# Performance work log

Measured on AMD Instinct MI355X. Metric: run time of the kernel, lower is better.

Reference implementation:

```python
import jax, jax.numpy as jnp
import numpy as np

NDIR = 6      # build_tree.num_directions()
IDIM = 256
ODIM = 512
B, L, NCH = 8, 4096, 8192


def setup_inputs() -> dict:
    key = jax.random.key(0)
    ks = jax.random.split(key, 9)
    last = jax.random.normal(ks[0], (B, NCH, IDIM), dtype=jnp.float32)
    child_l = jax.random.randint(ks[1], (L,), 0, NCH, dtype=jnp.int32)
    child_r = jax.random.randint(ks[2], (L,), 0, NCH, dtype=jnp.int32)
    vec = jax.random.randint(ks[3], (B, L), 0, NCH, dtype=jnp.int32)
    drev = jax.random.randint(ks[4], (NCH,), 0, 2, dtype=jnp.int32)
    dmap = jax.random.randint(ks[5], (NCH,), 0, NDIR, dtype=jnp.int32)
    # merge FC params: ndir independent Linear(2*idim -> odim) + PReLU(init=relu_weight)
    scale = 1.0 / np.sqrt(2 * IDIM)
    W_merge = jax.random.uniform(ks[6], (NDIR, ODIM, 2 * IDIM), jnp.float32, -scale, scale)
    b_merge = jax.random.uniform(ks[7], (NDIR, ODIM), jnp.float32, -scale, scale)
    alpha_merge = jnp.full((NDIR,), 0.005, dtype=jnp.float32)  # PReLU weight (relu_weight)
    return {"last": last, "W_merge": W_merge, "b_merge": b_merge,
            "alpha_merge": alpha_merge, "child_l": child_l, "child_r": child_r,
            "vec": vec, "drev": drev, "dmap": dmap}


def reference(last, W_merge, b_merge, alpha_merge, child_l, child_r, vec, drev, dmap):
    # child gathers: [B, L, idim]
    lch = last[:, child_l]
    rch = last[:, child_r]
    # per-element direction-reverse blending
    d = drev[vec][:, :, None].astype(last.dtype)          # [B, L, 1]
    a = lch * (1.0 - d) + rch * d
    b = rch * (1.0 - d) + lch * d
    ans = jnp.concatenate([a, b], axis=-1)                # [B, L, 2*idim]
    # routed merge: compute all ndir linears, then select per element (ndir is small)
    y_all = jnp.einsum('bli,doi->bldo', ans, W_merge) + b_merge   # [B, L, ndir, odim]
    dir_idx = dmap[vec]                                   # [B, L] in [0, ndir)
    y = jnp.take_along_axis(y_all, dir_idx[:, :, None, None], axis=2)[:, :, 0]  # [B, L, odim]
    alpha = alpha_merge[dir_idx][:, :, None]              # per-element PReLU slope
    return jnp.where(y > 0, y, alpha * y)
```

## Files before the change

kernel.cpp:

```cpp
#include <hip/hip_runtime.h>
#include <hip/hip_bf16.h>

#define BB 8
#define LL 4096
#define NCH 8192
#define IDIM 256
#define KDIM 512
#define ODIM 512
#define NDIR 6
#define TOT (BB * LL)
#define MT 64

typedef short short8 __attribute__((ext_vector_type(8)));
typedef float floatx4 __attribute__((ext_vector_type(4)));

#define IDX_OFF 64
#define ROWS_OFF (64 + NDIR * TOT)
#define LASTBF_OFF (64 + 2 * NDIR * TOT)
#define LAST_ELEMS (BB * NCH * IDIM)
#define W_ELEMS (NDIR * ODIM * KDIM)
#define N_LAST8 (LAST_ELEMS / 8)
#define N_W8 (W_ELEMS / 8)

__device__ inline void async_copy16(const void* g, void* l) {
  __builtin_amdgcn_global_load_lds(
      (const __attribute__((address_space(1))) void*)g,
      (__attribute__((address_space(3))) void*)l, 16, 0, 0);
}

__device__ inline void cvt8(const float* __restrict__ src,
                            __hip_bfloat16* __restrict__ dst, int i) {
  const floatx4* s = (const floatx4*)src;
  floatx4 a = s[2 * i];
  floatx4 b = s[2 * i + 1];
  union { short8 v; __hip_bfloat16 h[8]; } u;
  u.h[0] = __float2bfloat16(a[0]); u.h[1] = __float2bfloat16(a[1]);
  u.h[2] = __float2bfloat16(a[2]); u.h[3] = __float2bfloat16(a[3]);
  u.h[4] = __float2bfloat16(b[0]); u.h[5] = __float2bfloat16(b[1]);
  u.h[6] = __float2bfloat16(b[2]); u.h[7] = __float2bfloat16(b[3]);
  ((short8*)dst)[i] = u.v;
}

__global__ __launch_bounds__(256) void scatter_kernel(
    const int* __restrict__ vec, const int* __restrict__ child_l,
    const int* __restrict__ child_r, const int* __restrict__ drev,
    const int* __restrict__ dmap, int* __restrict__ ws) {
  __shared__ int lcnt[8];
  __shared__ int gbase[8];
  int tid = threadIdx.x;
  if (tid < 8) lcnt[tid] = 0;
  __syncthreads();

  int t = blockIdx.x * 256 + tid;
  int l = t & (LL - 1);
  int v = vec[t];
  int dir = dmap[v] & 7;
  int sw = drev[v];
  int cl = child_l[l];
  int cr = child_r[l];
  int r0 = sw ? cr : cl;
  int r1 = sw ? cl : cr;
  int pos = atomicAdd(&lcnt[dir], 1);
  __syncthreads();
  if (tid < 8) gbase[tid] = lcnt[tid] ? atomicAdd(&ws[tid], lcnt[tid]) : 0;
  __syncthreads();
  int slot = dir * TOT + gbase[dir] + pos;
  ws[IDX_OFF + slot] = t;
  ws[ROWS_OFF + slot] = r0 | (r1 << 16);
}

__global__ __launch_bounds__(256) void prep_kernel(
    const float* __restrict__ last, const float* __restrict__ W,
    int* __restrict__ ws) {
  __hip_bfloat16* last_bf = (__hip_bfloat16*)(ws + LASTBF_OFF);
  __hip_bfloat16* W_bf = last_bf + LAST_ELEMS;
  int gid = blockIdx.x * 256 + threadIdx.x;
  if (gid < N_LAST8) cvt8(last, last_bf, gid);
  else cvt8(W, W_bf, gid - N_LAST8);
}

__global__ __launch_bounds__(256) void gemm_kernel(
    const float* __restrict__ bias, const float* __restrict__ alpha_m,
    const int* __restrict__ ws, float* __restrict__ out) {
  __shared__ __hip_bfloat16 Als[2][MT * 32];
  __shared__ __hip_bfloat16 Bls[2][128 * 32];

  const int mt = blockIdx.y;
  const int nt = blockIdx.x;
  int d = -1, count = 0, m_base = 0;
  {
    int tb = 0;
    for (int dd = 0; dd < NDIR; ++dd) {
      int c = ws[dd];
      int ntile = (c + MT - 1) / MT;
      if (mt < tb + ntile) { d = dd; count = c; m_base = (mt - tb) * MT; break; }
      tb += ntile;
    }
  }
  if (d < 0) return;

  const __hip_bfloat16* last_bf = (const __hip_bfloat16*)(ws + LASTBF_OFF);
  const __hip_bfloat16* W_bf = last_bf + LAST_ELEMS;
  const int* idx = ws + IDX_OFF + d * TOT;
  const int* rows = ws + ROWS_OFF + d * TOT;

  const int tid = threadIdx.x;
  const int wave = __builtin_amdgcn_readfirstlane(tid >> 6);
  const int lane = tid & 63;
  const int lane15 = lane & 15;
  const int quad = lane >> 4;
  const int wm = wave >> 1;
  const int wn = wave & 1;
  const int n_blk = nt * 128;

  const int su = ((tid & 3) ^ ((tid >> 3) & 3)) * 8;
  const __hip_bfloat16* pa0;
  const __hip_bfloat16* pa1;
  {
    int r = tid >> 2;
    int lr = m_base + r;
    if (lr >= count) lr = count - 1;
    int t = idx[lr] & (TOT - 1);
    int rr = rows[lr];
    int b = t >> 12;
    int r0 = rr & (NCH - 1);
    int r1 = (rr >> 16) & (NCH - 1);
    pa0 = last_bf + (long long)(b * NCH + r0) * IDIM + su;
    pa1 = last_bf + (long long)(b * NCH + r1) * IDIM + su;
  }
  const __hip_bfloat16* pb[2];
#pragma unroll
  for (int i = 0; i < 2; ++i) {
    int rB = i * 64 + (tid >> 2);
    pb[i] = W_bf + (long long)(d * ODIM + n_blk + rB) * KDIM + su;
  }
  const int aBase = wave * 512;
  const int bBase0 = wave * 512;
  const int bBase1 = 2048 + wave * 512;

  floatx4 acc[2][4] = {};
  const int xcol = (quad ^ ((lane15 >> 1) & 3)) * 8;

  {
    async_copy16(pa0, &Als[0][aBase]);
    async_copy16(pb[0], &Bls[0][bBase0]);
    async_copy16(pb[1], &Bls[0][bBase1]);
  }

#pragma unroll
  for (int kt = 0; kt < 16; ++kt) {
    __syncthreads();
    if (kt < 15) {
      const int nb = (kt + 1) & 1;
      const int kn = kt + 1;
      const __hip_bfloat16* ga = (kn < 8) ? pa0 + kn * 32 : pa1 + (kn - 8) * 32;
      async_copy16(ga, &Als[nb][aBase]);
      async_copy16(pb[0] + kn * 32, &Bls[nb][bBase0]);
      async_copy16(pb[1] + kn * 32, &Bls[nb][bBase1]);
    }
    const int c = kt & 1;
    short8 a[2], b[4];
#pragma unroll
    for (int i = 0; i < 2; ++i)
      a[i] = *(const short8*)&Als[c][(wm * 32 + i * 16 + lane15) * 32 + xcol];
#pragma unroll
    for (int j = 0; j < 4; ++j)
      b[j] = *(const short8*)&Bls[c][(wn * 64 + j * 16 + lane15) * 32 + xcol];
#pragma unroll
    for (int i = 0; i < 2; ++i)
#pragma unroll
      for (int j = 0; j < 4; ++j)
        acc[i][j] = __builtin_amdgcn_mfma_f32_16x16x32_bf16(a[i], b[j], acc[i][j], 0, 0, 0);
  }

  const float alpha = alpha_m[d];
  float bj[4];
#pragma unroll
  for (int j = 0; j < 4; ++j)
    bj[j] = bias[d * ODIM + n_blk + wn * 64 + j * 16 + lane15];

#pragma unroll
  for (int i = 0; i < 2; ++i) {
#pragma unroll
    for (int reg = 0; reg < 4; ++reg) {
      int row_id = m_base + wm * 32 + i * 16 + quad * 4 + reg;
      if (row_id >= count) continue;
      int t = idx[row_id] & (TOT - 1);
      float* orow = out + (long long)t * ODIM + n_blk + wn * 64;
#pragma unroll
      for (int j = 0; j < 4; ++j) {
        float y = acc[i][j][reg] + bj[j];
        y = y > 0.f ? y : alpha * y;
        orow[j * 16 + lane15] = y;
      }
    }
  }
}

extern "C" void kernel_launch(void* const* d_in, const int* in_sizes, int n_in,
                              void* d_out, int out_size, void* d_ws, size_t ws_size,
                              hipStream_t stream) {
  const float* last = (const float*)d_in[0];
  const float* W = (const float*)d_in[1];
  const float* bias = (const float*)d_in[2];
  const float* alpha = (const float*)d_in[3];
  const int* child_l = (const int*)d_in[4];
  const int* child_r = (const int*)d_in[5];
  const int* vec = (const int*)d_in[6];
  const int* drev = (const int*)d_in[7];
  const int* dmap = (const int*)d_in[8];

  int* ws = (int*)d_ws;

  hipMemsetAsync(ws, 0, 32, stream);
  scatter_kernel<<<TOT / 256, 256, 0, stream>>>(vec, child_l, child_r, drev, dmap, ws);
  prep_kernel<<<(N_LAST8 + N_W8) / 256, 256, 0, stream>>>(last, W, ws);
  dim3 grid(ODIM / 128, TOT / MT + NDIR, 1);
  gemm_kernel<<<grid, 256, 0, stream>>>(bias, alpha, ws, (float*)d_out);
}
```

Before: 173.5 us.

## Convert gathered fp32 rows to bf16 in-register; drop full last conversion pass

Removes the pre-pass that converted the whole 64M-element `last` tensor to bf16. The GEMM now gathers fp32 child rows straight from global memory into registers and converts them to bf16 before the MFMA. B fragments are likewise loaded directly from global into registers with double buffering, replacing the LDS staging and barriers. The scatter and weight-conversion kernels are merged into one launch. The cost is twice the bytes per gathered A element, and each wave redundantly loads A and B without LDS sharing, which adds global/L2 traffic.

```diff
diff --git a/kernel.cpp b/kernel.cpp
--- a/kernel.cpp
+++ b/kernel.cpp
@@ -16,75 +16,57 @@
 
 #define IDX_OFF 64
 #define ROWS_OFF (64 + NDIR * TOT)
-#define LASTBF_OFF (64 + 2 * NDIR * TOT)
-#define LAST_ELEMS (BB * NCH * IDIM)
+#define WBF_OFF (64 + 2 * NDIR * TOT)
 #define W_ELEMS (NDIR * ODIM * KDIM)
-#define N_LAST8 (LAST_ELEMS / 8)
 #define N_W8 (W_ELEMS / 8)
 
-__device__ inline void async_copy16(const void* g, void* l) {
-  __builtin_amdgcn_global_load_lds(
-      (const __attribute__((address_space(1))) void*)g,
-      (__attribute__((address_space(3))) void*)l, 16, 0, 0);
-}
-
-__device__ inline void cvt8(const float* __restrict__ src,
-                            __hip_bfloat16* __restrict__ dst, int i) {
-  const floatx4* s = (const floatx4*)src;
-  floatx4 a = s[2 * i];
-  floatx4 b = s[2 * i + 1];
-  union { short8 v; __hip_bfloat16 h[8]; } u;
-  u.h[0] = __float2bfloat16(a[0]); u.h[1] = __float2bfloat16(a[1]);
-  u.h[2] = __float2bfloat16(a[2]); u.h[3] = __float2bfloat16(a[3]);
-  u.h[4] = __float2bfloat16(b[0]); u.h[5] = __float2bfloat16(b[1]);
-  u.h[6] = __float2bfloat16(b[2]); u.h[7] = __float2bfloat16(b[3]);
-  ((short8*)dst)[i] = u.v;
-}
-
-__global__ __launch_bounds__(256) void scatter_kernel(
+__global__ __launch_bounds__(256) void prep_kernel(
     const int* __restrict__ vec, const int* __restrict__ child_l,
     const int* __restrict__ child_r, const int* __restrict__ drev,
-    const int* __restrict__ dmap, int* __restrict__ ws) {
-  __shared__ int lcnt[8];
-  __shared__ int gbase[8];
+    const int* __restrict__ dmap, const float* __restrict__ W,
+    int* __restrict__ ws) {
+  int bid = blockIdx.x;
   int tid = threadIdx.x;
-  if (tid < 8) lcnt[tid] = 0;
-  __syncthreads();
-
-  int t = blockIdx.x * 256 + tid;
-  int l = t & (LL - 1);
-  int v = vec[t];
-  int dir = dmap[v] & 7;
-  int sw = drev[v];
-  int cl = child_l[l];
-  int cr = child_r[l];
-  int r0 = sw ? cr : cl;
-  int r1 = sw ? cl : cr;
-  int pos = atomicAdd(&lcnt[dir], 1);
-  __syncthreads();
-  if (tid < 8) gbase[tid] = lcnt[tid] ? atomicAdd(&ws[tid], lcnt[tid]) : 0;
-  __syncthreads();
-  int slot = dir * TOT + gbase[dir] + pos;
-  ws[IDX_OFF + slot] = t;
-  ws[ROWS_OFF + slot] = r0 | (r1 << 16);
+  if (bid < TOT / 256) {
+    __shared__ int lcnt[8];
+    __shared__ int gbase[8];
+    if (tid < 8) lcnt[tid] = 0;
+    __syncthreads();
+    int t = bid * 256 + tid;
+    int l = t & (LL - 1);
+    int v = vec[t];
+    int dir = dmap[v] & 7;
+    int sw = drev[v];
+    int cl = child_l[l];
+    int cr = child_r[l];
+    int r0 = sw ? cr : cl;
+    int r1 = sw ? cl : cr;
+    int pos = atomicAdd(&lcnt[dir], 1);
+    __syncthreads();
+    if (tid < 8) gbase[tid] = lcnt[tid] ? atomicAdd(&ws[tid], lcnt[tid]) : 0;
+    __syncthreads();
+    int slot = dir * TOT + gbase[dir] + pos;
+    ws[IDX_OFF + slot] = t;
+    ws[ROWS_OFF + slot] = r0 | (r1 << 16);
+  } else {
+    int gid = (bid - TOT / 256) * 256 + tid;
+    __hip_bfloat16* W_bf = (__hip_bfloat16*)(ws + WBF_OFF);
+    const floatx4* s = (const floatx4*)W;
+    floatx4 a = s[2 * gid];
+    floatx4 b = s[2 * gid + 1];
+    union { short8 v; __hip_bfloat16 h[8]; } u;
+    u.h[0] = __float2bfloat16(a[0]); u.h[1] = __float2bfloat16(a[1]);
+    u.h[2] = __float2bfloat16(a[2]); u.h[3] = __float2bfloat16(a[3]);
+    u.h[4] = __float2bfloat16(b[0]); u.h[5] = __float2bfloat16(b[1]);
+    u.h[6] = __float2bfloat16(b[2]); u.h[7] = __float2bfloat16(b[3]);
+    ((short8*)W_bf)[gid] = u.v;
+  }
 }
 
-__global__ __launch_bounds__(256) void prep_kernel(
-    const float* __restrict__ last, const float* __restrict__ W,
-    int* __restrict__ ws) {
-  __hip_bfloat16* last_bf = (__hip_bfloat16*)(ws + LASTBF_OFF);
-  __hip_bfloat16* W_bf = last_bf + LAST_ELEMS;
-  int gid = blockIdx.x * 256 + threadIdx.x;
-  if (gid < N_LAST8) cvt8(last, last_bf, gid);
-  else cvt8(W, W_bf, gid - N_LAST8);
-}
-
 __global__ __launch_bounds__(256) void gemm_kernel(
-    const float* __restrict__ bias, const float* __restrict__ alpha_m,
-    const int* __restrict__ ws, float* __restrict__ out) {
-  __shared__ __hip_bfloat16 Als[2][MT * 32];
-  __shared__ __hip_bfloat16 Bls[2][128 * 32];
-
+    const float* __restrict__ last, const float* __restrict__ bias,
+    const float* __restrict__ alpha_m, const int* __restrict__ ws,
+    float* __restrict__ out) {
   const int mt = blockIdx.y;
   const int nt = blockIdx.x;
   int d = -1, count = 0, m_base = 0;
@@ -99,8 +81,7 @@
   }
   if (d < 0) return;
 
-  const __hip_bfloat16* last_bf = (const __hip_bfloat16*)(ws + LASTBF_OFF);
-  const __hip_bfloat16* W_bf = last_bf + LAST_ELEMS;
+  const __hip_bfloat16* W_bf = (const __hip_bfloat16*)(ws + WBF_OFF);
   const int* idx = ws + IDX_OFF + d * TOT;
   const int* rows = ws + ROWS_OFF + d * TOT;
 
@@ -113,64 +94,70 @@
   const int wn = wave & 1;
   const int n_blk = nt * 128;
 
-  const int su = ((tid & 3) ^ ((tid >> 3) & 3)) * 8;
-  const __hip_bfloat16* pa0;
-  const __hip_bfloat16* pa1;
-  {
-    int r = tid >> 2;
-    int lr = m_base + r;
+  const float* paf0[2];
+  const float* paf1[2];
+#pragma unroll
+  for (int i = 0; i < 2; ++i) {
+    int lr = m_base + wm * 32 + i * 16 + lane15;
     if (lr >= count) lr = count - 1;
     int t = idx[lr] & (TOT - 1);
     int rr = rows[lr];
     int b = t >> 12;
     int r0 = rr & (NCH - 1);
     int r1 = (rr >> 16) & (NCH - 1);
-    pa0 = last_bf + (long long)(b * NCH + r0) * IDIM + su;
-    pa1 = last_bf + (long long)(b * NCH + r1) * IDIM + su;
-  }
-  const __hip_bfloat16* pb[2];
+    paf0[i] = last + (long long)(b * NCH + r0) * IDIM + quad * 8;
+    paf1[i] = last + (long long)(b * NCH + r1) * IDIM + quad * 8;
+  }
+  const __hip_bfloat16* pb[4];
+#pragma unroll
+  for (int j = 0; j < 4; ++j)
+    pb[j] = W_bf + (long long)(d * ODIM + n_blk + wn * 64 + j * 16 + lane15) * KDIM + quad * 8;
+
+  floatx4 acc[2][4] = {};
+
+  floatx4 ar[2][2][2];
+  short8 br[2][4];
+
 #pragma unroll
   for (int i = 0; i < 2; ++i) {
-    int rB = i * 64 + (tid >> 2);
-    pb[i] = W_bf + (long long)(d * ODIM + n_blk + rB) * KDIM + su;
-  }
-  const int aBase = wave * 512;
-  const int bBase0 = wave * 512;
-  const int bBase1 = 2048 + wave * 512;
-
-  floatx4 acc[2][4] = {};
-  const int xcol = (quad ^ ((lane15 >> 1) & 3)) * 8;
-
-  {
-    async_copy16(pa0, &Als[0][aBase]);
-    async_copy16(pb[0], &Bls[0][bBase0]);
-    async_copy16(pb[1], &Bls[0][bBase1]);
-  }
+    ar[0][i][0] = *(const floatx4*)(paf0[i]);
+    ar[0][i][1] = *(const floatx4*)(paf0[i] + 4);
+  }
+#pragma unroll
+  for (int j = 0; j < 4; ++j) br[0][j] = *(const short8*)(pb[j]);
 
 #pragma unroll
   for (int kt = 0; kt < 16; ++kt) {
-    __syncthreads();
+    const int cur = kt & 1;
+    const int nxt = cur ^ 1;
     if (kt < 15) {
-      const int nb = (kt + 1) & 1;
       const int kn = kt + 1;
-      const __hip_bfloat16* ga = (kn < 8) ? pa0 + kn * 32 : pa1 + (kn - 8) * 32;
-      async_copy16(ga, &Als[nb][aBase]);
-      async_copy16(pb[0] + kn * 32, &Bls[nb][bBase0]);
-      async_copy16(pb[1] + kn * 32, &Bls[nb][bBase1]);
-    }
-    const int c = kt & 1;
-    short8 a[2], b[4];
+#pragma unroll
+      for (int i = 0; i < 2; ++i) {
+        const float* p = (kn < 8) ? paf0[i] + kn * 32 : paf1[i] + (kn - 8) * 32;
+        ar[nxt][i][0] = *(const floatx4*)(p);
+        ar[nxt][i][1] = *(const floatx4*)(p + 4);
+      }
+#pragma unroll
+      for (int j = 0; j < 4; ++j) br[nxt][j] = *(const short8*)(pb[j] + kn * 32);
+    }
+    short8 a[2];
+#pragma unroll
+    for (int i = 0; i < 2; ++i) {
+      union { short8 v; __hip_bfloat16 h[8]; } u;
+      floatx4 x0 = ar[cur][i][0];
+      floatx4 x1 = ar[cur][i][1];
+      u.h[0] = __float2bfloat16(x0[0]); u.h[1] = __float2bfloat16(x0[1]);
+      u.h[2] = __float2bfloat16(x0[2]); u.h[3] = __float2bfloat16(x0[3]);
+      u.h[4] = __float2bfloat16(x1[0]); u.h[5] = __float2bfloat16(x1[1]);
+      u.h[6] = __float2bfloat16(x1[2]); u.h[7] = __float2bfloat16(x1[3]);
+      a[i] = u.v;
+    }
 #pragma unroll
     for (int i = 0; i < 2; ++i)
-      a[i] = *(const short8*)&Als[c][(wm * 32 + i * 16 + lane15) * 32 + xcol];
-#pragma unroll
-    for (int j = 0; j < 4; ++j)
-      b[j] = *(const short8*)&Bls[c][(wn * 64 + j * 16 + lane15) * 32 + xcol];
-#pragma unroll
-    for (int i = 0; i < 2; ++i)
 #pragma unroll
       for (int j = 0; j < 4; ++j)
-        acc[i][j] = __builtin_amdgcn_mfma_f32_16x16x32_bf16(a[i], b[j], acc[i][j], 0, 0, 0);
+        acc[i][j] = __builtin_amdgcn_mfma_f32_16x16x32_bf16(a[i], br[cur][j], acc[i][j], 0, 0, 0);
   }
 
   const float alpha = alpha_m[d];
@@ -213,8 +200,8 @@
   int* ws = (int*)d_ws;
 
   hipMemsetAsync(ws, 0, 32, stream);
-  scatter_kernel<<<TOT / 256, 256, 0, stream>>>(vec, child_l, child_r, drev, dmap, ws);
-  prep_kernel<<<(N_LAST8 + N_W8) / 256, 256, 0, stream>>>(last, W, ws);
+  prep_kernel<<<TOT / 256 + N_W8 / 256, 256, 0, stream>>>(
+      vec, child_l, child_r, drev, dmap, W, ws);
   dim3 grid(ODIM / 128, TOT / MT + NDIR, 1);
-  gemm_kernel<<<grid, 256, 0, stream>>>(bias, alpha, ws, (float*)d_out);
+  gemm_kernel<<<grid, 256, 0, stream>>>(last, bias, alpha, ws, (float*)d_out);
 }
```

Result: slower. 252.3 us (+45.5%).

## Enlarge GEMM tile to 128x128 with K=64 steps and fuse scatter into prep kernel

Applied to the files above, without the earlier changes.

The grouped GEMM tile grows from 64x128 to 128x128, and each K step is now 64 wide with an 8-way XOR swizzle. This doubles operand reuse per LDS load and halves the number of barriers per tile. Separately, the scatter and bf16-conversion kernels are merged into one launch using block-range dispatch, which removes one kernel launch. The cost is more LDS and accumulator registers per block, which can lower occupancy, plus more padding waste on the partial last tile of each direction.

```diff
diff --git a/kernel.cpp b/kernel.cpp
--- a/kernel.cpp
+++ b/kernel.cpp
@@ -9,7 +9,7 @@
 #define ODIM 512
 #define NDIR 6
 #define TOT (BB * LL)
-#define MT 64
+#define MT 128
 
 typedef short short8 __attribute__((ext_vector_type(8)));
 typedef float floatx4 __attribute__((ext_vector_type(4)));
@@ -21,6 +21,9 @@
 #define W_ELEMS (NDIR * ODIM * KDIM)
 #define N_LAST8 (LAST_ELEMS / 8)
 #define N_W8 (W_ELEMS / 8)
+#define SCAT_BLK (TOT / 256)
+#define CVTL_BLK (N_LAST8 / 256)
+#define CVTW_BLK (N_W8 / 256)
 
 __device__ inline void async_copy16(const void* g, void* l) {
   __builtin_amdgcn_global_load_lds(
@@ -41,49 +44,48 @@
   ((short8*)dst)[i] = u.v;
 }
 
-__global__ __launch_bounds__(256) void scatter_kernel(
+__global__ __launch_bounds__(256) void prep_kernel(
     const int* __restrict__ vec, const int* __restrict__ child_l,
     const int* __restrict__ child_r, const int* __restrict__ drev,
-    const int* __restrict__ dmap, int* __restrict__ ws) {
-  __shared__ int lcnt[8];
-  __shared__ int gbase[8];
-  int tid = threadIdx.x;
-  if (tid < 8) lcnt[tid] = 0;
-  __syncthreads();
-
-  int t = blockIdx.x * 256 + tid;
-  int l = t & (LL - 1);
-  int v = vec[t];
-  int dir = dmap[v] & 7;
-  int sw = drev[v];
-  int cl = child_l[l];
-  int cr = child_r[l];
-  int r0 = sw ? cr : cl;
-  int r1 = sw ? cl : cr;
-  int pos = atomicAdd(&lcnt[dir], 1);
-  __syncthreads();
-  if (tid < 8) gbase[tid] = lcnt[tid] ? atomicAdd(&ws[tid], lcnt[tid]) : 0;
-  __syncthreads();
-  int slot = dir * TOT + gbase[dir] + pos;
-  ws[IDX_OFF + slot] = t;
-  ws[ROWS_OFF + slot] = r0 | (r1 << 16);
-}
-
-__global__ __launch_bounds__(256) void prep_kernel(
-    const float* __restrict__ last, const float* __restrict__ W,
-    int* __restrict__ ws) {
+    const int* __restrict__ dmap, const float* __restrict__ last,
+    const float* __restrict__ W, int* __restrict__ ws) {
   __hip_bfloat16* last_bf = (__hip_bfloat16*)(ws + LASTBF_OFF);
   __hip_bfloat16* W_bf = last_bf + LAST_ELEMS;
-  int gid = blockIdx.x * 256 + threadIdx.x;
-  if (gid < N_LAST8) cvt8(last, last_bf, gid);
-  else cvt8(W, W_bf, gid - N_LAST8);
-}
-
-__global__ __launch_bounds__(256) void gemm_kernel(
+  int bid = blockIdx.x;
+  int tid = threadIdx.x;
+  if (bid < SCAT_BLK) {
+    __shared__ int lcnt[8];
+    __shared__ int gbase[8];
+    if (tid < 8) lcnt[tid] = 0;
+    __syncthreads();
+    int t = bid * 256 + tid;
+    int l = t & (LL - 1);
+    int v = vec[t];
+    int dir = dmap[v] & 7;
+    int sw = drev[v];
+    int cl = child_l[l];
+    int cr = child_r[l];
+    int r0 = sw ? cr : cl;
+    int r1 = sw ? cl : cr;
+    int pos = atomicAdd(&lcnt[dir], 1);
+    __syncthreads();
+    if (tid < 8) gbase[tid] = lcnt[tid] ? atomicAdd(&ws[tid], lcnt[tid]) : 0;
+    __syncthreads();
+    int slot = dir * TOT + gbase[dir] + pos;
+    ws[IDX_OFF + slot] = t;
+    ws[ROWS_OFF + slot] = r0 | (r1 << 16);
+  } else if (bid < SCAT_BLK + CVTL_BLK) {
+    cvt8(last, last_bf, (bid - SCAT_BLK) * 256 + tid);
+  } else {
+    cvt8(W, W_bf, (bid - SCAT_BLK - CVTL_BLK) * 256 + tid);
+  }
+}
+
+__global__ __launch_bounds__(256, 2) void gemm_kernel(
     const float* __restrict__ bias, const float* __restrict__ alpha_m,
     const int* __restrict__ ws, float* __restrict__ out) {
-  __shared__ __hip_bfloat16 Als[2][MT * 32];
-  __shared__ __hip_bfloat16 Bls[2][128 * 32];
+  __shared__ __hip_bfloat16 Als[2][128 * 64];
+  __shared__ __hip_bfloat16 Bls[2][128 * 64];
 
   const int mt = blockIdx.y;
   const int nt = blockIdx.x;
@@ -113,64 +115,67 @@
   const int wn = wave & 1;
   const int n_blk = nt * 128;
 
-  const int su = ((tid & 3) ^ ((tid >> 3) & 3)) * 8;
-  const __hip_bfloat16* pa0;
-  const __hip_bfloat16* pa1;
-  {
-    int r = tid >> 2;
-    int lr = m_base + r;
+  const __hip_bfloat16* ap0[4];
+  const __hip_bfloat16* ap1[4];
+  const __hip_bfloat16* bp[4];
+  int ldsrow[4];
+#pragma unroll
+  for (int i = 0; i < 4; ++i) {
+    int sr = wave * 32 + i * 8 + (lane >> 3);
+    ldsrow[i] = (wave * 32 + i * 8) * 64;
+    int lr = m_base + sr;
     if (lr >= count) lr = count - 1;
     int t = idx[lr] & (TOT - 1);
     int rr = rows[lr];
     int b = t >> 12;
     int r0 = rr & (NCH - 1);
     int r1 = (rr >> 16) & (NCH - 1);
-    pa0 = last_bf + (long long)(b * NCH + r0) * IDIM + su;
-    pa1 = last_bf + (long long)(b * NCH + r1) * IDIM + su;
-  }
-  const __hip_bfloat16* pb[2];
-#pragma unroll
-  for (int i = 0; i < 2; ++i) {
-    int rB = i * 64 + (tid >> 2);
-    pb[i] = W_bf + (long long)(d * ODIM + n_blk + rB) * KDIM + su;
-  }
-  const int aBase = wave * 512;
-  const int bBase0 = wave * 512;
-  const int bBase1 = 2048 + wave * 512;
-
-  floatx4 acc[2][4] = {};
-  const int xcol = (quad ^ ((lane15 >> 1) & 3)) * 8;
-
-  {
-    async_copy16(pa0, &Als[0][aBase]);
-    async_copy16(pb[0], &Bls[0][bBase0]);
-    async_copy16(pb[1], &Bls[0][bBase1]);
-  }
-
-#pragma unroll
-  for (int kt = 0; kt < 16; ++kt) {
-    __syncthreads();
-    if (kt < 15) {
-      const int nb = (kt + 1) & 1;
+    int xu = ((lane & 7) ^ (sr & 7)) * 8;
+    ap0[i] = last_bf + (long long)(b * NCH + r0) * IDIM + xu;
+    ap1[i] = last_bf + (long long)(b * NCH + r1) * IDIM + xu;
+    bp[i] = W_bf + (long long)(d * ODIM + n_blk + sr) * KDIM + xu;
+  }
+
+  floatx4 acc[4][4] = {};
+  const int lx = lane15 & 7;
+
+#pragma unroll
+  for (int i = 0; i < 4; ++i) {
+    async_copy16(ap0[i], &Als[0][ldsrow[i]]);
+    async_copy16(bp[i], &Bls[0][ldsrow[i]]);
+  }
+
+#pragma unroll
+  for (int kt = 0; kt < 8; ++kt) {
+    __syncthreads();
+    if (kt < 7) {
       const int kn = kt + 1;
-      const __hip_bfloat16* ga = (kn < 8) ? pa0 + kn * 32 : pa1 + (kn - 8) * 32;
-      async_copy16(ga, &Als[nb][aBase]);
-      async_copy16(pb[0] + kn * 32, &Bls[nb][bBase0]);
-      async_copy16(pb[1] + kn * 32, &Bls[nb][bBase1]);
+      const int nb = kn & 1;
+      const int ko = (kn & 3) * 64;
+#pragma unroll
+      for (int i = 0; i < 4; ++i) {
+        const __hip_bfloat16* ga = (kn < 4 ? ap0[i] : ap1[i]) + ko;
+        async_copy16(ga, &Als[nb][ldsrow[i]]);
+        async_copy16(bp[i] + kn * 64, &Bls[nb][ldsrow[i]]);
+      }
     }
     const int c = kt & 1;
-    short8 a[2], b[4];
-#pragma unroll
-    for (int i = 0; i < 2; ++i)
-      a[i] = *(const short8*)&Als[c][(wm * 32 + i * 16 + lane15) * 32 + xcol];
-#pragma unroll
-    for (int j = 0; j < 4; ++j)
-      b[j] = *(const short8*)&Bls[c][(wn * 64 + j * 16 + lane15) * 32 + xcol];
-#pragma unroll
-    for (int i = 0; i < 2; ++i)
+#pragma unroll
+    for (int s = 0; s < 2; ++s) {
+      const int xcol = ((quad + 4 * s) ^ lx) * 8;
+      short8 a[4], b[4];
+#pragma unroll
+      for (int i = 0; i < 4; ++i)
+        a[i] = *(const short8*)&Als[c][(wm * 64 + i * 16 + lane15) * 64 + xcol];
 #pragma unroll
       for (int j = 0; j < 4; ++j)
-        acc[i][j] = __builtin_amdgcn_mfma_f32_16x16x32_bf16(a[i], b[j], acc[i][j], 0, 0, 0);
+        b[j] = *(const short8*)&Bls[c][(wn * 64 + j * 16 + lane15) * 64 + xcol];
+#pragma unroll
+      for (int i = 0; i < 4; ++i)
+#pragma unroll
+        for (int j = 0; j < 4; ++j)
+          acc[i][j] = __builtin_amdgcn_mfma_f32_16x16x32_bf16(a[i], b[j], acc[i][j], 0, 0, 0);
+    }
   }
 
   const float alpha = alpha_m[d];
@@ -180,10 +185,10 @@
     bj[j] = bias[d * ODIM + n_blk + wn * 64 + j * 16 + lane15];
 
 #pragma unroll
-  for (int i = 0; i < 2; ++i) {
+  for (int i = 0; i < 4; ++i) {
 #pragma unroll
     for (int reg = 0; reg < 4; ++reg) {
-      int row_id = m_base + wm * 32 + i * 16 + quad * 4 + reg;
+      int row_id = m_base + wm * 64 + i * 16 + quad * 4 + reg;
       if (row_id >= count) continue;
       int t = idx[row_id] & (TOT - 1);
       float* orow = out + (long long)t * ODIM + n_blk + wn * 64;
@@ -213,8 +218,8 @@
   int* ws = (int*)d_ws;
 
   hipMemsetAsync(ws, 0, 32, stream);
-  scatter_kernel<<<TOT / 256, 256, 0, stream>>>(vec, child_l, child_r, drev, dmap, ws);
-  prep_kernel<<<(N_LAST8 + N_W8) / 256, 256, 0, stream>>>(last, W, ws);
+  prep_kernel<<<SCAT_BLK + CVTL_BLK + CVTW_BLK, 256, 0, stream>>>(
+      vec, child_l, child_r, drev, dmap, last, W, ws);
   dim3 grid(ODIM / 128, TOT / MT + NDIR, 1);
   gemm_kernel<<<grid, 256, 0, stream>>>(bias, alpha, ws, (float*)d_out);
 }
```

After: 173.9 us. About the same (+0.2%).
